# Kernel tuning notes

Hardware: AMD Instinct MI355X
Metric: run time of the kernel (lower is better)

Reference implementation:

```python
import jax, jax.numpy as jnp
from jax import lax
import numpy as np

I, H, O, T, B = 13, 64, 13, 5, 262144


def setup_inputs() -> dict:
    key = jax.random.key(0)
    ks = jax.random.split(key, 10)
    s = 1.0 / np.sqrt(H)  # pytorch LSTM/Linear init scale
    x = jax.random.normal(ks[0], (B, T, I), dtype=jnp.float32)
    W_ih = jax.random.uniform(ks[1], (4 * H, I), jnp.float32, -s, s)
    W_hh = jax.random.uniform(ks[2], (4 * H, H), jnp.float32, -s, s)
    b_ih = jax.random.uniform(ks[3], (4 * H,), jnp.float32, -s, s)
    b_hh = jax.random.uniform(ks[4], (4 * H,), jnp.float32, -s, s)
    W1 = jax.random.uniform(ks[5], (H, H), jnp.float32, -s, s)
    b1 = jax.random.uniform(ks[6], (H,), jnp.float32, -s, s)
    W2 = jax.random.uniform(ks[7], (O, H), jnp.float32, -s, s)
    b2 = jax.random.uniform(ks[8], (O,), jnp.float32, -s, s)
    return {"x": x, "W_ih": W_ih, "W_hh": W_hh, "b_ih": b_ih, "b_hh": b_hh,
            "W1": W1, "b1": b1, "W2": W2, "b2": b2}


def _lstm_last_hidden(x, W_ih, W_hh, b_ih, b_hh):
    # Precompute input contributions for all timesteps: [B, T, 4H]
    xg = jnp.einsum('bti,gi->btg', x, W_ih) + b_ih + b_hh
    h0 = jnp.zeros((x.shape[0], H), x.dtype)

    def step(carry, xt):
        h, c = carry
        g = xt + h @ W_hh.T  # [B, 4H], gate order: i, f, g, o
        i, f, gg, o = jnp.split(g, 4, axis=-1)
        c = jax.nn.sigmoid(f) * c + jax.nn.sigmoid(i) * jnp.tanh(gg)
        h = jax.nn.sigmoid(o) * jnp.tanh(c)
        return (h, c), None

    (h, _), _ = lax.scan(step, (h0, h0), jnp.swapaxes(xg, 0, 1))
    return h  # last timestep hidden == lstm_output[:, -1, :]


def reference(x, W_ih, W_hh, b_ih, b_hh, W1, b1, W2, b2):
    h = _lstm_last_hidden(x, W_ih, W_hh, b_ih, b_hh)
    z = jax.nn.relu(h @ W1.T + b1)  # dropout=0.0 -> identity
    return z @ W2.T + b2  # [B, O]
```

## Files before the change

kernel.cpp:

```cpp
#include <hip/hip_runtime.h>
#include <math.h>


#define TT 5
#define NI 13

typedef _Float16 half8 __attribute__((ext_vector_type(8)));
typedef __attribute__((ext_vector_type(4))) float f32x4;
typedef __attribute__((ext_vector_type(2))) float f32x2;

#define WHH_OFF  0
#define WIH_OFF  32768
#define W1_OFF   40960
#define W2_OFF   49152
#define BIAS_OFF 51200

#define LOG2E 1.44269504088896340736f
#define TWO_LOG2E 2.88539008177792681472f

__device__ __forceinline__ float gate_scale(int n) {
  return ((n >> 6) == 2) ? TWO_LOG2E : -LOG2E;
}

__device__ __forceinline__ f32x2 vexp2(f32x2 v) {
  f32x2 r;
  r[0] = __builtin_amdgcn_exp2f(v[0]);
  r[1] = __builtin_amdgcn_exp2f(v[1]);
  return r;
}
__device__ __forceinline__ f32x2 vrcp(f32x2 v) {
  f32x2 r;
  r[0] = __builtin_amdgcn_rcpf(v[0]);
  r[1] = __builtin_amdgcn_rcpf(v[1]);
  return r;
}

__global__ void prep_kernel(const float* __restrict__ W_ih,
                            const float* __restrict__ W_hh,
                            const float* __restrict__ b_ih,
                            const float* __restrict__ b_hh,
                            const float* __restrict__ W1,
                            const float* __restrict__ W2,
                            _Float16* __restrict__ whh,
                            _Float16* __restrict__ wih,
                            _Float16* __restrict__ w1,
                            _Float16* __restrict__ w2,
                            float* __restrict__ bias) {
  int idx = blockIdx.x * 256 + threadIdx.x;
  if (idx < 16384) {
    int kt = idx >> 13, r = idx & 8191;
    int nt = r >> 9, lane = (r >> 3) & 63, j = idx & 7;
    int k = kt * 32 + ((lane >> 4) << 3) + j;
    int n = (nt << 4) + (lane & 15);
    whh[idx] = (_Float16)(W_hh[n * 64 + k] * gate_scale(n));
  }
  if (idx < 4096) {
    int nt = idx >> 8, l32 = (idx >> 3) & 31, j = idx & 7;
    int k = ((l32 >> 4) << 3) + j;
    int n = (nt << 4) + (l32 & 15);
    wih[idx] = (_Float16)((k < NI) ? W_ih[n * NI + k] * gate_scale(n) : 0.f);
  }
  if (idx < 4096) {
    int kt = idx >> 11, r = idx & 2047;
    int nt = r >> 9, lane = (r >> 3) & 63, j = idx & 7;
    int k = kt * 32 + ((lane >> 4) << 3) + j;
    int n = (nt << 4) + (lane & 15);
    w1[idx] = (_Float16)W1[n * 64 + k];
  }
  if (idx < 1024) {
    int kt = idx >> 9, lane = (idx >> 3) & 63, j = idx & 7;
    int k = kt * 32 + ((lane >> 4) << 3) + j;
    int n = lane & 15;
    w2[idx] = (_Float16)((n < 13) ? W2[n * 64 + k] : 0.f);
  }
  if (idx < 256) bias[idx] = (b_ih[idx] + b_hh[idx]) * gate_scale(idx);
}

__device__ __forceinline__ void read_afrags(const _Float16* __restrict__ hw,
                                            int quad, int mcol, half8 a[2][2]) {
#pragma unroll
  for (int mt = 0; mt < 2; ++mt) {
    const int r = mt * 16 + mcol;
#pragma unroll
    for (int kt = 0; kt < 2; ++kt) {
      const int blk = (kt * 4 + quad) ^ (r & 7);
      a[mt][kt] = *(const half8*)&hw[r * 64 + blk * 8];
    }
  }
}

__global__ __launch_bounds__(512, 4)
void lstm_mfma(const float* __restrict__ x,
               const _Float16* __restrict__ wm_g,
               const _Float16* __restrict__ w1_g,
               const _Float16* __restrict__ w2_g,
               const float* __restrict__ biasp,
               const float* __restrict__ b1v,
               const float* __restrict__ b2v,
               float* __restrict__ out) {
  __shared__ __attribute__((aligned(16))) _Float16 wlds[20480];
  __shared__ __attribute__((aligned(16))) _Float16 hshm[8][2048];

  const int tid = threadIdx.x;
  const int wave = tid >> 6;
  const int lane = tid & 63;
  const int quad = lane >> 4;
  const int mcol = lane & 15;
  _Float16* __restrict__ hw = &hshm[wave][0];
  const int row0 = blockIdx.x * 256 + wave * 32;

  {
    const f32x4* __restrict__ s = (const f32x4*)wm_g;
    f32x4* d = (f32x4*)wlds;
#pragma unroll
    for (int i = 0; i < 5; ++i) d[tid + 512 * i] = s[tid + 512 * i];
  }
  __syncthreads();

  f32x2 c_st[2][4][2];
#pragma unroll
  for (int mt = 0; mt < 2; ++mt)
#pragma unroll
    for (int jt = 0; jt < 4; ++jt)
#pragma unroll
      for (int p = 0; p < 2; ++p) { c_st[mt][jt][p][0] = 0.f; c_st[mt][jt][p][1] = 0.f; }

  float bias_r[4][4];
#pragma unroll
  for (int g = 0; g < 4; ++g)
#pragma unroll
    for (int jt = 0; jt < 4; ++jt)
      bias_r[g][jt] = biasp[((g * 4 + jt) << 4) + mcol];

  const half8* __restrict__ whhf = (const half8*)wlds;
  const half8* __restrict__ wihf = (const half8*)(wlds + 16384);

#pragma unroll 1
  for (int t = 0; t < TT; ++t) {
    half8 xa[2];
#pragma unroll
    for (int mt = 0; mt < 2; ++mt) {
      const float* __restrict__ xp =
          x + (size_t)(row0 + mt * 16 + mcol) * (TT * NI) + t * NI;
      half8 v;
#pragma unroll
      for (int j = 0; j < 8; ++j) v[j] = (_Float16)0.f;
      if (quad == 0) {
        float lo[4], hi[4];
        __builtin_memcpy(lo, xp, 16);
        __builtin_memcpy(hi, xp + 4, 16);
#pragma unroll
        for (int j = 0; j < 4; ++j) {
          v[j] = (_Float16)lo[j];
          v[4 + j] = (_Float16)hi[j];
        }
      } else if (quad == 1) {
        float lo[4];
        __builtin_memcpy(lo, xp + 8, 16);
        const float e12 = xp[12];
#pragma unroll
        for (int j = 0; j < 4; ++j) v[j] = (_Float16)lo[j];
        v[4] = (_Float16)e12;
      }
      xa[mt] = v;
    }

    half8 ah[2][2];
    if (t > 0) read_afrags(hw, quad, mcol, ah);

#pragma unroll 1
    for (int jt = 0; jt < 4; ++jt) {
      f32x4 acc[2][4];
#pragma unroll
      for (int mt = 0; mt < 2; ++mt)
#pragma unroll
        for (int g = 0; g < 4; ++g) {
          const float b = bias_r[g][jt];
          f32x4 z = {b, b, b, b};
          acc[mt][g] = z;
        }

#pragma unroll
      for (int g = 0; g < 4; ++g) {
        const half8 bfr = wihf[(g * 4 + jt) * 32 + (lane & 31)];
#pragma unroll
        for (int mt = 0; mt < 2; ++mt)
          acc[mt][g] = __builtin_amdgcn_mfma_f32_16x16x32_f16(xa[mt], bfr, acc[mt][g], 0, 0, 0);
      }

      if (t > 0) {
#pragma unroll
        for (int kt = 0; kt < 2; ++kt)
#pragma unroll
          for (int g = 0; g < 4; ++g) {
            const half8 bfr = whhf[(kt * 16 + g * 4 + jt) * 64 + lane];
#pragma unroll
            for (int mt = 0; mt < 2; ++mt)
              acc[mt][g] = __builtin_amdgcn_mfma_f32_16x16x32_f16(ah[mt][kt], bfr, acc[mt][g], 0, 0, 0);
          }
      }

#pragma unroll
      for (int mt = 0; mt < 2; ++mt)
#pragma unroll
        for (int p = 0; p < 2; ++p) {
          f32x2 si = {acc[mt][0][p * 2], acc[mt][0][p * 2 + 1]};
          f32x2 sf = {acc[mt][1][p * 2], acc[mt][1][p * 2 + 1]};
          f32x2 sg = {acc[mt][2][p * 2], acc[mt][2][p * 2 + 1]};
          f32x2 so = {acc[mt][3][p * 2], acc[mt][3][p * 2 + 1]};
          const f32x2 A  = vexp2(sf);
          const f32x2 Bv = vexp2(si);
          const f32x2 E  = vexp2(sg);
          const f32x2 pA = 1.f + A;
          const f32x2 pB = 1.f + Bv;
          const f32x2 ep = E + 1.f;
          const f32x2 em = E - 1.f;
          const f32x2 m1 = pB * ep;
          f32x2 cv = c_st[mt][jt][p];
          const f32x2 num = cv * m1 + em * pA;
          cv = num * vrcp(pA * m1);
          c_st[mt][jt][p] = cv;
          const f32x2 C2 = vexp2(so);
          const f32x2 F  = vexp2(cv * TWO_LOG2E);
          const f32x2 hn = (F - 1.f) * vrcp((1.f + C2) * (F + 1.f));
#pragma unroll
          for (int u = 0; u < 2; ++u) {
            const int r = mt * 16 + quad * 4 + p * 2 + u;
            const int k = jt * 16 + mcol;
            hw[r * 64 + (((k >> 3) ^ (r & 7)) << 3) + (k & 7)] = (_Float16)hn[u];
          }
        }
    }
  }

  {
    half8 ah[2][2];
    read_afrags(hw, quad, mcol, ah);

    f32x4 zacc[2][4];
#pragma unroll
    for (int nt = 0; nt < 4; ++nt) {
      const float b = b1v[nt * 16 + mcol];
#pragma unroll
      for (int mt = 0; mt < 2; ++mt) {
        f32x4 z = {b, b, b, b};
        zacc[mt][nt] = z;
      }
    }
#pragma unroll
    for (int kt = 0; kt < 2; ++kt)
#pragma unroll
      for (int nt = 0; nt < 4; ++nt) {
        const half8 bfr = ((const half8*)w1_g)[(kt * 4 + nt) * 64 + lane];
#pragma unroll
        for (int mt = 0; mt < 2; ++mt)
          zacc[mt][nt] = __builtin_amdgcn_mfma_f32_16x16x32_f16(ah[mt][kt], bfr, zacc[mt][nt], 0, 0, 0);
      }
#pragma unroll
    for (int mt = 0; mt < 2; ++mt)
#pragma unroll
      for (int nt = 0; nt < 4; ++nt)
#pragma unroll
        for (int reg = 0; reg < 4; ++reg) {
          const float zv = fmaxf(zacc[mt][nt][reg], 0.f);
          const int r = mt * 16 + quad * 4 + reg;
          const int k = nt * 16 + mcol;
          hw[r * 64 + (((k >> 3) ^ (r & 7)) << 3) + (k & 7)] = (_Float16)zv;
        }
  }

  {
    half8 zh[2][2];
    read_afrags(hw, quad, mcol, zh);

    const float b2r = (mcol < 13) ? b2v[mcol] : 0.f;
    f32x4 oacc[2];
#pragma unroll
    for (int mt = 0; mt < 2; ++mt) {
      f32x4 z = {b2r, b2r, b2r, b2r};
      oacc[mt] = z;
    }
#pragma unroll
    for (int kt = 0; kt < 2; ++kt) {
      const half8 bfr = ((const half8*)w2_g)[kt * 64 + lane];
#pragma unroll
      for (int mt = 0; mt < 2; ++mt)
        oacc[mt] = __builtin_amdgcn_mfma_f32_16x16x32_f16(zh[mt][kt], bfr, oacc[mt], 0, 0, 0);
    }
    if (mcol < 13) {
#pragma unroll
      for (int mt = 0; mt < 2; ++mt)
#pragma unroll
        for (int reg = 0; reg < 4; ++reg) {
          const int row = row0 + mt * 16 + quad * 4 + reg;
          out[row * 13 + mcol] = oacc[mt][reg];
        }
    }
  }
}

extern "C" void kernel_launch(void* const* d_in, const int* in_sizes, int n_in,
                              void* d_out, int out_size, void* d_ws, size_t ws_size,
                              hipStream_t stream) {
  const float* x    = (const float*)d_in[0];
  const float* W_ih = (const float*)d_in[1];
  const float* W_hh = (const float*)d_in[2];
  const float* b_ih = (const float*)d_in[3];
  const float* b_hh = (const float*)d_in[4];
  const float* W1   = (const float*)d_in[5];
  const float* b1   = (const float*)d_in[6];
  const float* W2   = (const float*)d_in[7];
  const float* b2   = (const float*)d_in[8];
  float* out = (float*)d_out;
  char* ws = (char*)d_ws;

  _Float16* whh = (_Float16*)(ws + WHH_OFF);
  _Float16* wih = (_Float16*)(ws + WIH_OFF);
  _Float16* w1  = (_Float16*)(ws + W1_OFF);
  _Float16* w2  = (_Float16*)(ws + W2_OFF);
  float* bias   = (float*)(ws + BIAS_OFF);

  hipLaunchKernelGGL(prep_kernel, dim3(64), dim3(256), 0, stream,
                     W_ih, W_hh, b_ih, b_hh, W1, W2, whh, wih, w1, w2, bias);

  const int B = in_sizes[0] / (TT * NI);
  hipLaunchKernelGGL(lstm_mfma, dim3(B / 256), dim3(512), 0, stream,
                     x, whh, w1, w2, bias, b1, b2, out);
}
```

Baseline: 222.7 us.

## Fold gate bias into input MFMA via constant-one columns and prefetch x

The combined LSTM gate bias moves into the padded K columns of the input weight fragment. A hi/lo fp16 split keeps precision, and the x fragment gets constant 1.0 entries in those columns. This drops the per-lane bias registers and the per-tile accumulator initialisation, so the input MFMAs now start from zero. The next timestep's x loads are also issued before the current step's compute, to hide global load latency behind the recurrent work. Register pressure drops for the bias but rises for the prefetched x values.

Measured after the change: 220.1 us. About the same (-1.2%).

```diff
diff --git a/kernel.cpp b/kernel.cpp
--- a/kernel.cpp
+++ b/kernel.cpp
@@ -13,7 +13,6 @@
 #define WIH_OFF  32768
 #define W1_OFF   40960
 #define W2_OFF   49152
-#define BIAS_OFF 51200
 
 #define LOG2E 1.44269504088896340736f
 #define TWO_LOG2E 2.88539008177792681472f
@@ -44,8 +43,7 @@
                             _Float16* __restrict__ whh,
                             _Float16* __restrict__ wih,
                             _Float16* __restrict__ w1,
-                            _Float16* __restrict__ w2,
-                            float* __restrict__ bias) {
+                            _Float16* __restrict__ w2) {
   int idx = blockIdx.x * 256 + threadIdx.x;
   if (idx < 16384) {
     int kt = idx >> 13, r = idx & 8191;
@@ -58,7 +56,16 @@
     int nt = idx >> 8, l32 = (idx >> 3) & 31, j = idx & 7;
     int k = ((l32 >> 4) << 3) + j;
     int n = (nt << 4) + (l32 & 15);
-    wih[idx] = (_Float16)((k < NI) ? W_ih[n * NI + k] * gate_scale(n) : 0.f);
+    float v = 0.f;
+    if (k < NI) {
+      v = W_ih[n * NI + k] * gate_scale(n);
+    } else if (k == NI) {
+      v = (b_ih[n] + b_hh[n]) * gate_scale(n);
+    } else if (k == NI + 1) {
+      float b = (b_ih[n] + b_hh[n]) * gate_scale(n);
+      v = b - (float)(_Float16)b;
+    }
+    wih[idx] = (_Float16)v;
   }
   if (idx < 4096) {
     int kt = idx >> 11, r = idx & 2047;
@@ -73,7 +80,6 @@
     int n = lane & 15;
     w2[idx] = (_Float16)((n < 13) ? W2[n * 64 + k] : 0.f);
   }
-  if (idx < 256) bias[idx] = (b_ih[idx] + b_hh[idx]) * gate_scale(idx);
 }
 
 __device__ __forceinline__ void read_afrags(const _Float16* __restrict__ hw,
@@ -94,7 +100,6 @@
                const _Float16* __restrict__ wm_g,
                const _Float16* __restrict__ w1_g,
                const _Float16* __restrict__ w2_g,
-               const float* __restrict__ biasp,
                const float* __restrict__ b1v,
                const float* __restrict__ b2v,
                float* __restrict__ out) {
@@ -125,44 +130,56 @@
 #pragma unroll
       for (int p = 0; p < 2; ++p) { c_st[mt][jt][p][0] = 0.f; c_st[mt][jt][p][1] = 0.f; }
 
-  float bias_r[4][4];
-#pragma unroll
-  for (int g = 0; g < 4; ++g)
-#pragma unroll
-    for (int jt = 0; jt < 4; ++jt)
-      bias_r[g][jt] = biasp[((g * 4 + jt) << 4) + mcol];
-
   const half8* __restrict__ whhf = (const half8*)wlds;
   const half8* __restrict__ wihf = (const half8*)(wlds + 16384);
 
+  const f32x4 ZERO4 = {0.f, 0.f, 0.f, 0.f};
+
+  const float* __restrict__ xp0 = x + (size_t)(row0 + mcol) * (TT * NI);
+  const float* __restrict__ xp1 = x + (size_t)(row0 + 16 + mcol) * (TT * NI);
+
+  f32x4 ra0, rb0, ra1, rb1;
+  if (quad == 0) {
+    __builtin_memcpy(&ra0, xp0, 16);  __builtin_memcpy(&rb0, xp0 + 4, 16);
+    __builtin_memcpy(&ra1, xp1, 16);  __builtin_memcpy(&rb1, xp1 + 4, 16);
+  } else if (quad == 1) {
+    __builtin_memcpy(&ra0, xp0 + 8, 16);  rb0[0] = xp0[12];
+    __builtin_memcpy(&ra1, xp1 + 8, 16);  rb1[0] = xp1[12];
+  }
+
 #pragma unroll 1
   for (int t = 0; t < TT; ++t) {
-    half8 xa[2];
-#pragma unroll
-    for (int mt = 0; mt < 2; ++mt) {
-      const float* __restrict__ xp =
-          x + (size_t)(row0 + mt * 16 + mcol) * (TT * NI) + t * NI;
-      half8 v;
-#pragma unroll
-      for (int j = 0; j < 8; ++j) v[j] = (_Float16)0.f;
+    half8 xa0, xa1;
+    {
+      half8 v0, v1;
+#pragma unroll
+      for (int j = 0; j < 8; ++j) { v0[j] = (_Float16)0.f; v1[j] = (_Float16)0.f; }
       if (quad == 0) {
-        float lo[4], hi[4];
-        __builtin_memcpy(lo, xp, 16);
-        __builtin_memcpy(hi, xp + 4, 16);
 #pragma unroll
         for (int j = 0; j < 4; ++j) {
-          v[j] = (_Float16)lo[j];
-          v[4 + j] = (_Float16)hi[j];
+          v0[j] = (_Float16)ra0[j]; v0[4 + j] = (_Float16)rb0[j];
+          v1[j] = (_Float16)ra1[j]; v1[4 + j] = (_Float16)rb1[j];
         }
       } else if (quad == 1) {
-        float lo[4];
-        __builtin_memcpy(lo, xp + 8, 16);
-        const float e12 = xp[12];
-#pragma unroll
-        for (int j = 0; j < 4; ++j) v[j] = (_Float16)lo[j];
-        v[4] = (_Float16)e12;
-      }
-      xa[mt] = v;
+#pragma unroll
+        for (int j = 0; j < 4; ++j) { v0[j] = (_Float16)ra0[j]; v1[j] = (_Float16)ra1[j]; }
+        v0[4] = (_Float16)rb0[0];  v1[4] = (_Float16)rb1[0];
+        v0[5] = (_Float16)1.f;     v1[5] = (_Float16)1.f;
+        v0[6] = (_Float16)1.f;     v1[6] = (_Float16)1.f;
+      }
+      xa0 = v0; xa1 = v1;
+    }
+
+    if (t + 1 < TT) {
+      const float* __restrict__ q0 = xp0 + (t + 1) * NI;
+      const float* __restrict__ q1 = xp1 + (t + 1) * NI;
+      if (quad == 0) {
+        __builtin_memcpy(&ra0, q0, 16);  __builtin_memcpy(&rb0, q0 + 4, 16);
+        __builtin_memcpy(&ra1, q1, 16);  __builtin_memcpy(&rb1, q1 + 4, 16);
+      } else if (quad == 1) {
+        __builtin_memcpy(&ra0, q0 + 8, 16);  rb0[0] = q0[12];
+        __builtin_memcpy(&ra1, q1 + 8, 16);  rb1[0] = q1[12];
+      }
     }
 
     half8 ah[2][2];
@@ -171,21 +188,12 @@
 #pragma unroll 1
     for (int jt = 0; jt < 4; ++jt) {
       f32x4 acc[2][4];
-#pragma unroll
-      for (int mt = 0; mt < 2; ++mt)
-#pragma unroll
-        for (int g = 0; g < 4; ++g) {
-          const float b = bias_r[g][jt];
-          f32x4 z = {b, b, b, b};
-          acc[mt][g] = z;
-        }
 
 #pragma unroll
       for (int g = 0; g < 4; ++g) {
         const half8 bfr = wihf[(g * 4 + jt) * 32 + (lane & 31)];
-#pragma unroll
-        for (int mt = 0; mt < 2; ++mt)
-          acc[mt][g] = __builtin_amdgcn_mfma_f32_16x16x32_f16(xa[mt], bfr, acc[mt][g], 0, 0, 0);
+        acc[0][g] = __builtin_amdgcn_mfma_f32_16x16x32_f16(xa0, bfr, ZERO4, 0, 0, 0);
+        acc[1][g] = __builtin_amdgcn_mfma_f32_16x16x32_f16(xa1, bfr, ZERO4, 0, 0, 0);
       }
 
       if (t > 0) {
@@ -318,12 +326,11 @@
   _Float16* wih = (_Float16*)(ws + WIH_OFF);
   _Float16* w1  = (_Float16*)(ws + W1_OFF);
   _Float16* w2  = (_Float16*)(ws + W2_OFF);
-  float* bias   = (float*)(ws + BIAS_OFF);
 
   hipLaunchKernelGGL(prep_kernel, dim3(64), dim3(256), 0, stream,
-                     W_ih, W_hh, b_ih, b_hh, W1, W2, whh, wih, w1, w2, bias);
+                     W_ih, W_hh, b_ih, b_hh, W1, W2, whh, wih, w1, w2);
 
   const int B = in_sizes[0] / (TT * NI);
   hipLaunchKernelGGL(lstm_mfma, dim3(B / 256), dim3(512), 0, stream,
-                     x, whh, w1, w2, bias, b1, b2, out);
-}
+                     x, whh, w1, w2, b1, b2, out);
+}
```
